# Kernel tuning notes

Measured on AMD Instinct MI355X. Metric: run time of the kernel, lower is better.

## Reference

```python
import jax, jax.numpy as jnp
import numpy as np

H, D = 8, 16            # num_heads, head_size
IN = H * D              # hgt_in_dim = 128
NT, ET = 3, 4           # node types, edge types (hard-coded in module)
N_DRUG, N_DIS, N_PROT = 10000, 10000, 30000
N = N_DRUG + N_DIS + N_PROT
E = 400000
LAYERS = 2
SQRT_D = float(np.sqrt(D))

# homogeneous node-type vector (presorted by type, as dgl.to_homogeneous yields)
NTYPE = jnp.concatenate([
    jnp.zeros(N_DRUG, jnp.int32),
    jnp.ones(N_DIS, jnp.int32),
    jnp.full((N_PROT,), 2, jnp.int32),
])


def typed_linear(x, types, W):
    # x: (M, in), W: (T, in, out), types: (M,) -> y[m] = x[m] @ W[types[m]]
    out = jnp.zeros((x.shape[0], W.shape[2]), x.dtype)
    for t in range(W.shape[0]):
        out = out + jnp.where((types == t)[:, None], x @ W[t], 0.0)
    return out


def hgt_conv(x, src, dst, etype, Wk, Wq, Wv, Wa, rel_att, rel_msg, pri, skip):
    # type-specific K/Q/V projections
    k = typed_linear(x, NTYPE, Wk).reshape(N, H, D)
    q = typed_linear(x, NTYPE, Wq).reshape(N, H, D)
    v = typed_linear(x, NTYPE, Wv).reshape(N, H, D)
    ke, qe, ve = k[src], q[dst], v[src]          # (E, H, D) gathers

    # per-edge-type relation transforms (vectorized over heads)
    kw = jnp.zeros_like(ke)
    mw = jnp.zeros_like(ve)
    for t in range(ET):
        sel = (etype == t)[:, None, None]
        kw = kw + jnp.where(sel, jnp.einsum('ehd,hdo->eho', ke, rel_att[:, t]), 0.0)
        mw = mw + jnp.where(sel, jnp.einsum('ehd,hdo->eho', ve, rel_msg[:, t]), 0.0)

    # attention logits: (kw . q) * relation_pri[head, etype] / sqrt(D)
    a = (kw * qe).sum(-1) * pri.T[etype] / SQRT_D  # (E, H)

    # edge softmax grouped by destination node, per head
    amax = jax.ops.segment_max(a, dst, num_segments=N)      # (N, H)
    ea = jnp.exp(a - amax[dst])
    esum = jax.ops.segment_sum(ea, dst, num_segments=N)
    attn = ea / esum[dst]                                   # (E, H)

    # weighted message aggregation (scatter-add over dst)
    m = mw * attn[..., None]                                 # (E, H, D)
    h = jax.ops.segment_sum(m, dst, num_segments=N).reshape(N, IN)

    # output projection (dropout = identity in eval) + sigmoid-skip residual
    h = typed_linear(h, NTYPE, Wa)
    alpha = jax.nn.sigmoid(skip)[NTYPE][:, None]
    return h * alpha + x * (1.0 - alpha)


def setup_inputs() -> dict:
    key = jax.random.key(0)
    ks = jax.random.split(key, 12)
    s = 0.05
    return {
        "drug_feature": jax.random.normal(ks[0], (N_DRUG, IN), jnp.float32),
        "disease_feature": jax.random.normal(ks[1], (N_DIS, IN), jnp.float32),
        "protein_feature": jax.random.normal(ks[2], (N_PROT, IN), jnp.float32),
        "src": jax.random.randint(ks[3], (E,), 0, N, dtype=jnp.int32),
        "dst": jax.random.randint(ks[4], (E,), 0, N, dtype=jnp.int32),
        "etype": jnp.sort(jax.random.randint(ks[5], (E,), 0, ET, dtype=jnp.int32)),
        "Wk": jax.random.normal(ks[6], (NT, IN, IN), jnp.float32) * s,
        "Wq": jax.random.normal(ks[7], (NT, IN, IN), jnp.float32) * s,
        "Wv": jax.random.normal(ks[8], (NT, IN, IN), jnp.float32) * s,
        "Wa": jax.random.normal(ks[9], (NT, IN, IN), jnp.float32) * s,
        "rel_att": jax.random.normal(ks[10], (H, ET, D, D), jnp.float32) * 0.1,
        "rel_msg": jax.random.normal(ks[11], (H, ET, D, D), jnp.float32) * 0.1,
        "pri": jnp.ones((H, ET), jnp.float32),
        "skip": jnp.ones((NT,), jnp.float32),
    }


def reference(drug_feature, disease_feature, protein_feature, src, dst, etype,
              Wk, Wq, Wv, Wa, rel_att, rel_msg, pri, skip):
    x = jnp.concatenate([drug_feature, disease_feature, protein_feature], axis=0)
    # ModuleList holds the SAME conv instance -> shared weights across layers
    for _ in range(LAYERS):
        x = hgt_conv(x, src, dst, etype, Wk, Wq, Wv, Wa, rel_att, rel_msg, pri, skip)
    return x
```

## Files before the change

### kernel.cpp

```cpp
#include <hip/hip_runtime.h>

#define N_NODE 50000
#define N_EDGE 400000
#define INF    128

#define FUSED_BLOCKS 1024

#define TILES0 313
#define TILES1 313
#define TILES2 938
#define PTILES 1564
#define PBLOCKS 391

#define SB_CONCAT 2048
#define SB_COUNT  1563
#define SB_TWT    768
#define SB_TRMSG  32
#define SB_TOTAL  (SB_CONCAT + SB_COUNT + SB_TWT + SB_TRMSG)

typedef __bf16 bf16x8 __attribute__((ext_vector_type(8)));
typedef float  f32x4  __attribute__((ext_vector_type(4)));

__device__ __forceinline__ void seg_decode(int b, int& ty, int& base, int& nrows) {
  if (b < TILES0)            { ty = 0; base = b * 32;                      nrows = 10000 - base; }
  else if (b < TILES0+TILES1){ ty = 1; base = 10000 + (b - TILES0) * 32;   nrows = 20000 - base; }
  else                       { ty = 2; base = 20000 + (b - TILES0-TILES1)*32; nrows = 50000 - base; }
  if (nrows > 32) nrows = 32;
}

__device__ __forceinline__ float blo(unsigned u) { return __uint_as_float(u << 16); }
__device__ __forceinline__ float bhi(unsigned u) { return __uint_as_float(u & 0xffff0000u); }
__device__ __forceinline__ unsigned bpack(float lo, float hi) {
  unsigned a = __float_as_uint(lo), b = __float_as_uint(hi);
  a = (a + 0x7fffu + ((a >> 16) & 1u)) >> 16;
  b = (b + 0x7fffu + ((b >> 16) & 1u)) & 0xffff0000u;
  return a | b;
}
__device__ __forceinline__ unsigned short b16(float v) {
  unsigned u = __float_as_uint(v);
  return (unsigned short)((u + 0x7fffu + ((u >> 16) & 1u)) >> 16);
}
__device__ __forceinline__ bf16x8 ld_frag(const unsigned short* p) {
  uint4 u = *reinterpret_cast<const uint4*>(p);
  return __builtin_bit_cast(bf16x8, u);
}

__global__ __launch_bounds__(256) void k_setup(const float* __restrict__ dr,
                                               const float* __restrict__ di,
                                               const float* __restrict__ pr,
                                               float* __restrict__ x,
                                               unsigned short* __restrict__ xh,
                                               const int* __restrict__ dst,
                                               int* __restrict__ deg,
                                               const float* __restrict__ Wk,
                                               const float* __restrict__ Wq,
                                               const float* __restrict__ Wv,
                                               const float* __restrict__ Wa,
                                               unsigned short* __restrict__ WT,
                                               const float* __restrict__ rm,
                                               float* __restrict__ AmT) {
  int b = blockIdx.x;
  if (b < SB_CONCAT) {
    for (int i = b * 256 + threadIdx.x; i < N_NODE * 32; i += SB_CONCAT * 256) {
      int row = i >> 5;
      float4 val;
      if (row < 10000)      val = ((const float4*)dr)[i];
      else if (row < 20000) val = ((const float4*)di)[i - 10000*32];
      else                  val = ((const float4*)pr)[i - 20000*32];
      ((float4*)x)[i] = val;
      ((uint2*)xh)[i] = make_uint2(bpack(val.x, val.y), bpack(val.z, val.w));
    }
  } else if (b < SB_CONCAT + SB_COUNT) {
    int e = (b - SB_CONCAT) * 256 + threadIdx.x;
    if (e < N_EDGE) atomicAdd(&deg[dst[e]], 1);
  } else if (b < SB_CONCAT + SB_COUNT + SB_TWT) {
    int idx = (b - SB_CONCAT - SB_COUNT) * 256 + threadIdx.x;
    if (idx < 196608) {
      int mt = idx >> 14;
      int within = idx & 16383;
      int o = within >> 7, ii = within & 127;
      int mat = mt / 3, ty = mt % 3;
      const float* W = (mat == 0) ? Wk : (mat == 1) ? Wq : (mat == 2) ? Wv : Wa;
      WT[idx] = b16(W[ty * 16384 + ii * 128 + o]);
    }
  } else {
    int i = (b - SB_CONCAT - SB_COUNT - SB_TWT) * 256 + threadIdx.x;
    int di2 = i & 15, doo = (i >> 4) & 15, ty = (i >> 8) & 3, hh = i >> 10;
    AmT[i] = rm[((hh * 4 + ty) * 16 + di2) * 16 + doo];
  }
}

__global__ __launch_bounds__(1024) void k_scan(const int* __restrict__ deg,
                                               int* __restrict__ off, int* __restrict__ cur) {
  __shared__ int part[1024];
  int t = threadIdx.x;
  int c0 = t * 49;
  int c1 = c0 + 49; if (c1 > N_NODE) c1 = N_NODE;
  int s = 0;
  for (int i = c0; i < c1; ++i) s += deg[i];
  part[t] = s;
  __syncthreads();
  for (int ofs = 1; ofs < 1024; ofs <<= 1) {
    int v = (t >= ofs) ? part[t - ofs] : 0;
    __syncthreads();
    part[t] += v;
    __syncthreads();
  }
  int run = (t == 0) ? 0 : part[t - 1];
  for (int i = c0; i < c1; ++i) { off[i] = run; cur[i] = run; run += deg[i]; }
  if (t == 1023) off[N_NODE] = part[1023];
}

__global__ __launch_bounds__(256) void k_fill(const int* __restrict__ dst,
                                              const int* __restrict__ src,
                                              const int* __restrict__ etp,
                                              int* __restrict__ cur, int* __restrict__ est) {
  int e = blockIdx.x * 256 + threadIdx.x;
  if (e < N_EDGE) {
    int p = atomicAdd(&cur[dst[e]], 1);
    est[p] = (src[e] << 2) | etp[e];
  } else if (e < N_EDGE + 64) {
    est[e] = 0;
  }
}

__global__ __launch_bounds__(256) void k_qkv(const unsigned short* __restrict__ xh,
                                             const unsigned short* __restrict__ WT,
                                             const float* __restrict__ rel_att,
                                             const float* __restrict__ pri,
                                             uint2* __restrict__ kvb,
                                             uint4* __restrict__ qab) {
  __shared__ unsigned short qsh[4][32][128];
  int w = threadIdx.x >> 6, l = threadIdx.x & 63;
  int r16 = l & 15, ks = l >> 4;
  int tile = blockIdx.x * 4 + w;
  int ty, base, wrows;
  seg_decode(tile, ty, base, wrows);
  int row0 = base;

  bf16x8 a[2][4];
#pragma unroll
  for (int st = 0; st < 2; ++st) {
    const unsigned short* xrow = xh + (size_t)(row0 + st * 16 + r16) * 128 + ks * 8;
#pragma unroll
    for (int kk = 0; kk < 4; ++kk) a[st][kk] = ld_frag(xrow + kk * 32);
  }

  const unsigned short* WK = WT + (size_t)(0 * 3 + ty) * 16384;
  const unsigned short* WQ = WT + (size_t)(1 * 3 + ty) * 16384;
  const unsigned short* WV = WT + (size_t)(2 * 3 + ty) * 16384;

#pragma unroll 1
  for (int ct = 0; ct < 8; ++ct) {
    int o = ct * 16 + r16;
    bf16x8 fbk[4], fbq[4], fbv[4];
#pragma unroll
    for (int kk = 0; kk < 4; ++kk) {
      fbk[kk] = ld_frag(WK + (size_t)o * 128 + ks * 8 + kk * 32);
      fbq[kk] = ld_frag(WQ + (size_t)o * 128 + ks * 8 + kk * 32);
      fbv[kk] = ld_frag(WV + (size_t)o * 128 + ks * 8 + kk * 32);
    }
#pragma unroll
    for (int st = 0; st < 2; ++st) {
      f32x4 ak = {0.f,0.f,0.f,0.f}, aq = {0.f,0.f,0.f,0.f}, av = {0.f,0.f,0.f,0.f};
#pragma unroll
      for (int kk = 0; kk < 4; ++kk) {
        ak = __builtin_amdgcn_mfma_f32_16x16x32_bf16(a[st][kk], fbk[kk], ak, 0, 0, 0);
        aq = __builtin_amdgcn_mfma_f32_16x16x32_bf16(a[st][kk], fbq[kk], aq, 0, 0, 0);
        av = __builtin_amdgcn_mfma_f32_16x16x32_bf16(a[st][kk], fbv[kk], av, 0, 0, 0);
      }
#pragma unroll
      for (int r = 0; r < 4; ++r) {
        int rrel = st * 16 + ks * 4 + r;
        float kn = __shfl_xor(ak[r], 1);
        float vn = __shfl_xor(av[r], 1);
        qsh[w][rrel][o] = b16(aq[r]);
        if (rrel < wrows && (l & 1) == 0) {
          size_t p = (size_t)(row0 + rrel);
          kvb[p * 64 + (o >> 1)] = make_uint2(bpack(ak[r], kn), bpack(av[r], vn));
        }
      }
    }
  }

  int h = l >> 3, j = l & 7;
  float4 prh = ((const float4*)pri)[h];
  float prs[4] = { prh.x * 0.25f, prh.y * 0.25f, prh.z * 0.25f, prh.w * 0.25f };
  for (int nd = 0; nd < wrows; ++nd) {
    unsigned u[8];
    *(uint4*)&u[0] = *(uint4*)&qsh[w][nd][h * 16 + 0];
    *(uint4*)&u[4] = *(uint4*)&qsh[w][nd][h * 16 + 8];
    float qf[16];
#pragma unroll
    for (int q2 = 0; q2 < 8; ++q2) { qf[2*q2] = blo(u[q2]); qf[2*q2+1] = bhi(u[q2]); }
    unsigned pk[4];
#pragma unroll
    for (int t4 = 0; t4 < 4; ++t4) {
      const float* Ar = rel_att + (((h * 4 + t4) * 16) + 2 * j) * 16;
      float ax = 0.f, ay = 0.f;
#pragma unroll
      for (int o = 0; o < 16; ++o) {
        ax += Ar[o] * qf[o];
        ay += Ar[16 + o] * qf[o];
      }
      pk[t4] = bpack(ax * prs[t4], ay * prs[t4]);
    }
    qab[(size_t)(row0 + nd) * 64 + l] = make_uint4(pk[0], pk[1], pk[2], pk[3]);
  }
}

__global__ __launch_bounds__(256)
__attribute__((amdgpu_waves_per_eu(4, 4)))
void k_fused(const uint2* __restrict__ kvb,
             const uint4* __restrict__ qab,
             const int* __restrict__ off,
             const int* __restrict__ est,
             const float* __restrict__ AmT,
             unsigned* __restrict__ hbh) {
  __shared__ float accs[4][4][128];
  int w = threadIdx.x >> 6, l = threadIdx.x & 63;
  int h = l >> 3, j = l & 7;

  for (int n = blockIdx.x * 4 + w; n < N_NODE; n += FUSED_BLOCKS * 4) {
    int o0 = off[n], o1 = off[n + 1];

    uint4 qu = qab[(size_t)n * 64 + l];
    float2 qa0 = make_float2(blo(qu.x), bhi(qu.x));
    float2 qa1 = make_float2(blo(qu.y), bhi(qu.y));
    float2 qa2 = make_float2(blo(qu.z), bhi(qu.z));
    float2 qa3 = make_float2(blo(qu.w), bhi(qu.w));

    float ssum = 0.f;
    float2 z = make_float2(0.f, 0.f);
    float2 at0 = z, at1 = z, at2 = z, at3 = z;

#define PROC(KV, TY, VALID) { \
    int ty = (TY) & 3; \
    float kx = blo((KV).x), ky = bhi((KV).x); \
    float2 qat = (ty==0)?qa0:(ty==1)?qa1:(ty==2)?qa2:qa3; \
    float part = kx*qat.x + ky*qat.y; \
    part += __shfl_xor(part, 1); \
    part += __shfl_xor(part, 2); \
    part += __shfl_xor(part, 4); \
    float wgt = (VALID) ? __expf(part) : 0.f; \
    ssum += wgt; \
    float vx = blo((KV).y), vy = bhi((KV).y); \
    float w0=(ty==0)?wgt:0.f, w1=(ty==1)?wgt:0.f, w2=(ty==2)?wgt:0.f, w3=(ty==3)?wgt:0.f; \
    at0.x += w0*vx; at0.y += w0*vy; \
    at1.x += w1*vx; at1.y += w1*vy; \
    at2.x += w2*vx; at2.y += w2*vy; \
    at3.x += w3*vx; at3.y += w3*vy; }

    for (int b0 = o0; b0 < o1; b0 += 64) {
      int cnt = o1 - b0; if (cnt > 64) cnt = 64;
      int stv = est[b0 + (l < cnt ? l : cnt - 1)];
      int t0 = __shfl(stv, 0);
      int t1 = __shfl(stv, 1 < cnt ? 1 : 0);
      uint2 kv0 = kvb[(size_t)(t0 >> 2) * 64 + l];
      uint2 kv1 = kvb[(size_t)(t1 >> 2) * 64 + l];
      for (int i = 0; i < cnt; i += 2) {
        bool more = (i + 2) < cnt;
        int n0 = 0, n1 = 0; uint2 kn0, kn1;
        if (more) {
          n0 = __shfl(stv, i + 2);
          n1 = __shfl(stv, (i + 3) < cnt ? (i + 3) : (i + 2));
          kn0 = kvb[(size_t)(n0 >> 2) * 64 + l];
          kn1 = kvb[(size_t)(n1 >> 2) * 64 + l];
        }
        PROC(kv0, t0, true)
        PROC(kv1, t1, (i + 1) < cnt)
        if (more) { t0 = n0; t1 = n1; kv0 = kn0; kv1 = kn1; }
      }
    }
#undef PROC

    float inv = (ssum > 0.f) ? 1.f / ssum : 0.f;
    at0.x *= inv; at0.y *= inv;
    at1.x *= inv; at1.y *= inv;
    at2.x *= inv; at2.y *= inv;
    at3.x *= inv; at3.y *= inv;

    ((float2*)&accs[w][0][0])[l] = at0;
    ((float2*)&accs[w][1][0])[l] = at1;
    ((float2*)&accs[w][2][0])[l] = at2;
    ((float2*)&accs[w][3][0])[l] = at3;

    float ox = 0.f, oy = 0.f;
#pragma unroll
    for (int ty = 0; ty < 4; ++ty) {
      const float4* AmR = (const float4*)(AmT + ((h * 4 + ty) * 16) * 16);
#pragma unroll
      for (int d4 = 0; d4 < 4; ++d4) {
        float4 ac = *((float4*)&accs[w][ty][h * 16 + d4 * 4]);
        float4 m0 = AmR[(2 * j) * 4 + d4];
        float4 m1 = AmR[(2 * j + 1) * 4 + d4];
        ox += m0.x * ac.x + m0.y * ac.y + m0.z * ac.z + m0.w * ac.w;
        oy += m1.x * ac.x + m1.y * ac.y + m1.z * ac.z + m1.w * ac.w;
      }
    }
    hbh[(size_t)n * 64 + l] = bpack(ox, oy);
  }
}

__global__ __launch_bounds__(256) void k_outqkv(const unsigned short* __restrict__ hbh,
                                                const unsigned short* __restrict__ WT,
                                                const float* __restrict__ skipv,
                                                const float* __restrict__ rel_att,
                                                const float* __restrict__ pri,
                                                float* __restrict__ xio,
                                                uint2* __restrict__ kvb,
                                                uint4* __restrict__ qab) {
  __shared__ unsigned short qsh[4][32][136];
  int w = threadIdx.x >> 6, l = threadIdx.x & 63;
  int r16 = l & 15, ks = l >> 4;
  int tile = blockIdx.x * 4 + w;
  int ty, base, wrows;
  seg_decode(tile, ty, base, wrows);
  int row0 = base;

  {
    bf16x8 a[2][4];
#pragma unroll
    for (int st = 0; st < 2; ++st) {
      const unsigned short* hrow = hbh + (size_t)(row0 + st * 16 + r16) * 128 + ks * 8;
#pragma unroll
      for (int kk = 0; kk < 4; ++kk) a[st][kk] = ld_frag(hrow + kk * 32);
    }
    const unsigned short* WA = WT + (size_t)(3 * 3 + ty) * 16384;
    float alpha = 1.f / (1.f + __expf(-skipv[ty]));
    float beta = 1.f - alpha;
#pragma unroll 1
    for (int ct = 0; ct < 8; ++ct) {
      int o = ct * 16 + r16;
      bf16x8 ba[4];
#pragma unroll
      for (int kk = 0; kk < 4; ++kk)
        ba[kk] = ld_frag(WA + (size_t)o * 128 + ks * 8 + kk * 32);
#pragma unroll
      for (int st = 0; st < 2; ++st) {
        f32x4 acc = {0.f,0.f,0.f,0.f};
#pragma unroll
        for (int kk = 0; kk < 4; ++kk)
          acc = __builtin_amdgcn_mfma_f32_16x16x32_bf16(a[st][kk], ba[kk], acc, 0, 0, 0);
#pragma unroll
        for (int r = 0; r < 4; ++r) {
          int rrel = st * 16 + ks * 4 + r;
          size_t p = (size_t)(row0 + rrel) * 128 + o;
          float nx = 0.f;
          if (rrel < wrows) {
            nx = acc[r] * alpha + xio[p] * beta;
            xio[p] = nx;
          }
          qsh[w][rrel][o] = b16(nx);
        }
      }
    }
  }

  bf16x8 a[2][4];
#pragma unroll
  for (int st = 0; st < 2; ++st)
#pragma unroll
    for (int kk = 0; kk < 4; ++kk)
      a[st][kk] = ld_frag(&qsh[w][st * 16 + r16][ks * 8 + kk * 32]);

  const unsigned short* WK = WT + (size_t)(0 * 3 + ty) * 16384;
  const unsigned short* WQ = WT + (size_t)(1 * 3 + ty) * 16384;
  const unsigned short* WV = WT + (size_t)(2 * 3 + ty) * 16384;
#pragma unroll 1
  for (int ct = 0; ct < 8; ++ct) {
    int o = ct * 16 + r16;
    bf16x8 fbk[4], fbq[4], fbv[4];
#pragma unroll
    for (int kk = 0; kk < 4; ++kk) {
      fbk[kk] = ld_frag(WK + (size_t)o * 128 + ks * 8 + kk * 32);
      fbq[kk] = ld_frag(WQ + (size_t)o * 128 + ks * 8 + kk * 32);
      fbv[kk] = ld_frag(WV + (size_t)o * 128 + ks * 8 + kk * 32);
    }
#pragma unroll
    for (int st = 0; st < 2; ++st) {
      f32x4 ak = {0.f,0.f,0.f,0.f}, aq = {0.f,0.f,0.f,0.f}, av = {0.f,0.f,0.f,0.f};
#pragma unroll
      for (int kk = 0; kk < 4; ++kk) {
        ak = __builtin_amdgcn_mfma_f32_16x16x32_bf16(a[st][kk], fbk[kk], ak, 0, 0, 0);
        aq = __builtin_amdgcn_mfma_f32_16x16x32_bf16(a[st][kk], fbq[kk], aq, 0, 0, 0);
        av = __builtin_amdgcn_mfma_f32_16x16x32_bf16(a[st][kk], fbv[kk], av, 0, 0, 0);
      }
#pragma unroll
      for (int r = 0; r < 4; ++r) {
        int rrel = st * 16 + ks * 4 + r;
        float kn = __shfl_xor(ak[r], 1);
        float vn = __shfl_xor(av[r], 1);
        qsh[w][rrel][o] = b16(aq[r]);
        if (rrel < wrows && (l & 1) == 0) {
          size_t p = (size_t)(row0 + rrel);
          kvb[p * 64 + (o >> 1)] = make_uint2(bpack(ak[r], kn), bpack(av[r], vn));
        }
      }
    }
  }

  int h = l >> 3, j = l & 7;
  float4 prh = ((const float4*)pri)[h];
  float prs[4] = { prh.x * 0.25f, prh.y * 0.25f, prh.z * 0.25f, prh.w * 0.25f };
  for (int nd = 0; nd < wrows; ++nd) {
    unsigned u[8];
    *(uint4*)&u[0] = *(uint4*)&qsh[w][nd][h * 16 + 0];
    *(uint4*)&u[4] = *(uint4*)&qsh[w][nd][h * 16 + 8];
    float qf[16];
#pragma unroll
    for (int q2 = 0; q2 < 8; ++q2) { qf[2*q2] = blo(u[q2]); qf[2*q2+1] = bhi(u[q2]); }
    unsigned pk[4];
#pragma unroll
    for (int t4 = 0; t4 < 4; ++t4) {
      const float* Ar = rel_att + (((h * 4 + t4) * 16) + 2 * j) * 16;
      float ax = 0.f, ay = 0.f;
#pragma unroll
      for (int o = 0; o < 16; ++o) {
        ax += Ar[o] * qf[o];
        ay += Ar[16 + o] * qf[o];
      }
      pk[t4] = bpack(ax * prs[t4], ay * prs[t4]);
    }
    qab[(size_t)(row0 + nd) * 64 + l] = make_uint4(pk[0], pk[1], pk[2], pk[3]);
  }
}

__global__ __launch_bounds__(256) void k_out(const unsigned short* __restrict__ hbh,
                                             const unsigned short* __restrict__ WT,
                                             const float* __restrict__ skipv,
                                             float* __restrict__ xio) {
  int w = threadIdx.x >> 6, l = threadIdx.x & 63;
  int r16 = l & 15, ks = l >> 4;
  int tile = blockIdx.x * 4 + w;
  int ty, base, wrows;
  seg_decode(tile, ty, base, wrows);
  int row0 = base;

  bf16x8 a[2][4];
#pragma unroll
  for (int st = 0; st < 2; ++st) {
    const unsigned short* hrow = hbh + (size_t)(row0 + st * 16 + r16) * 128 + ks * 8;
#pragma unroll
    for (int kk = 0; kk < 4; ++kk) a[st][kk] = ld_frag(hrow + kk * 32);
  }

  const unsigned short* WA = WT + (size_t)(3 * 3 + ty) * 16384;
  float alpha = 1.f / (1.f + __expf(-skipv[ty]));
  float beta = 1.f - alpha;

#pragma unroll 1
  for (int ct = 0; ct < 8; ++ct) {
    int o = ct * 16 + r16;
    bf16x8 ba[4];
#pragma unroll
    for (int kk = 0; kk < 4; ++kk)
      ba[kk] = ld_frag(WA + (size_t)o * 128 + ks * 8 + kk * 32);
#pragma unroll
    for (int st = 0; st < 2; ++st) {
      f32x4 acc = {0.f,0.f,0.f,0.f};
#pragma unroll
      for (int kk = 0; kk < 4; ++kk)
        acc = __builtin_amdgcn_mfma_f32_16x16x32_bf16(a[st][kk], ba[kk], acc, 0, 0, 0);
#pragma unroll
      for (int r = 0; r < 4; ++r) {
        int rrel = st * 16 + ks * 4 + r;
        if (rrel < wrows) {
          size_t p = (size_t)(row0 + rrel) * 128 + o;
          xio[p] = acc[r] * alpha + xio[p] * beta;
        }
      }
    }
  }
}

extern "C" void kernel_launch(void* const* d_in, const int* in_sizes, int n_in,
                              void* d_out, int out_size, void* d_ws, size_t ws_size,
                              hipStream_t stream) {
  const float* drug = (const float*)d_in[0];
  const float* dis  = (const float*)d_in[1];
  const float* prot = (const float*)d_in[2];
  const int* src    = (const int*)d_in[3];
  const int* dst    = (const int*)d_in[4];
  const int* etp    = (const int*)d_in[5];
  const float* Wk   = (const float*)d_in[6];
  const float* Wq   = (const float*)d_in[7];
  const float* Wv   = (const float*)d_in[8];
  const float* Wa   = (const float*)d_in[9];
  const float* rel_att = (const float*)d_in[10];
  const float* rel_msg = (const float*)d_in[11];
  const float* pri  = (const float*)d_in[12];
  const float* skip = (const float*)d_in[13];
  float* x = (float*)d_out;

  char* w = (char*)d_ws;
  uint2*          kvb = (uint2*)(w + 0);
  unsigned*       hbh = (unsigned*)(w + 25600000);
  uint4*          qab = (uint4*)(w + 38400000);
  unsigned short* xh  = (unsigned short*)(w + 89600000);
  unsigned short* WT  = (unsigned short*)(w + 102400000);
  float*          AmT = (float*)(w + 102793216);
  int*            off = (int*)(w + 102825984);
  int*            est = (int*)(w + 103026048);
  int*            deg = (int*)(w + 25600000);
  int*            cur = (int*)(w + 25800064);

  (void)hipMemsetAsync(deg, 0, N_NODE * sizeof(int), stream);
  k_setup<<<SB_TOTAL, 256, 0, stream>>>(drug, dis, prot, x, xh, dst, deg,
                                        Wk, Wq, Wv, Wa, WT, rel_msg, AmT);
  k_scan<<<1, 1024, 0, stream>>>(deg, off, cur);
  k_fill<<<(N_EDGE + 64 + 255) / 256, 256, 0, stream>>>(dst, src, etp, cur, est);

  k_qkv<<<PBLOCKS, 256, 0, stream>>>(xh, WT, rel_att, pri, kvb, qab);
  k_fused<<<FUSED_BLOCKS, 256, 0, stream>>>(kvb, qab, off, est, AmT, hbh);
  k_outqkv<<<PBLOCKS, 256, 0, stream>>>((const unsigned short*)hbh, WT, skip,
                                        rel_att, pri, x, kvb, qab);
  k_fused<<<FUSED_BLOCKS, 256, 0, stream>>>(kvb, qab, off, est, AmT, hbh);
  k_out<<<PBLOCKS, 256, 0, stream>>>((const unsigned short*)hbh, WT, skip, x);
}
```

Before: 779.8 us.

## Split each projection tile across two waves and double block count

The projection kernels (k_qkv, k_outqkv, k_out) now assign two waves per 32-row tile, each handling half of the output column tiles and half of the rows in the rel_att post-pass, coordinated through shared memory and __syncthreads. The grid doubles from 391 to 782 blocks, so a GPU with many compute units gets more parallel work on a 1564-tile problem. Each wave still loads the full A fragments, so some global loads are duplicated, and the new block barriers add synchronisation. The fused kernel's waves_per_eu hint is also relaxed from (4,4) to (3,4), giving the compiler more register freedom.

```diff
diff --git a/kernel.cpp b/kernel.cpp
--- a/kernel.cpp
+++ b/kernel.cpp
@@ -10,7 +10,7 @@
 #define TILES1 313
 #define TILES2 938
 #define PTILES 1564
-#define PBLOCKS 391
+#define PBLOCKS2 782
 
 #define SB_CONCAT 2048
 #define SB_COUNT  1563
@@ -130,10 +130,11 @@
                                              const float* __restrict__ pri,
                                              uint2* __restrict__ kvb,
                                              uint4* __restrict__ qab) {
-  __shared__ unsigned short qsh[4][32][128];
+  __shared__ unsigned short qsh[2][32][136];
   int w = threadIdx.x >> 6, l = threadIdx.x & 63;
   int r16 = l & 15, ks = l >> 4;
-  int tile = blockIdx.x * 4 + w;
+  int t = w >> 1, ch = w & 1;
+  int tile = blockIdx.x * 2 + t;
   int ty, base, wrows;
   seg_decode(tile, ty, base, wrows);
   int row0 = base;
@@ -151,7 +152,7 @@
   const unsigned short* WV = WT + (size_t)(2 * 3 + ty) * 16384;
 
 #pragma unroll 1
-  for (int ct = 0; ct < 8; ++ct) {
+  for (int ct = ch * 4; ct < ch * 4 + 4; ++ct) {
     int o = ct * 16 + r16;
     bf16x8 fbk[4], fbq[4], fbv[4];
 #pragma unroll
@@ -174,7 +175,7 @@
         int rrel = st * 16 + ks * 4 + r;
         float kn = __shfl_xor(ak[r], 1);
         float vn = __shfl_xor(av[r], 1);
-        qsh[w][rrel][o] = b16(aq[r]);
+        qsh[t][rrel][o] = b16(aq[r]);
         if (rrel < wrows && (l & 1) == 0) {
           size_t p = (size_t)(row0 + rrel);
           kvb[p * 64 + (o >> 1)] = make_uint2(bpack(ak[r], kn), bpack(av[r], vn));
@@ -182,14 +183,18 @@
       }
     }
   }
+  __syncthreads();
 
   int h = l >> 3, j = l & 7;
   float4 prh = ((const float4*)pri)[h];
   float prs[4] = { prh.x * 0.25f, prh.y * 0.25f, prh.z * 0.25f, prh.w * 0.25f };
-  for (int nd = 0; nd < wrows; ++nd) {
+  int nd0 = ch * 16;
+  int lim = wrows - nd0; if (lim > 16) lim = 16;
+  for (int i = 0; i < lim; ++i) {
+    int nd = nd0 + i;
     unsigned u[8];
-    *(uint4*)&u[0] = *(uint4*)&qsh[w][nd][h * 16 + 0];
-    *(uint4*)&u[4] = *(uint4*)&qsh[w][nd][h * 16 + 8];
+    *(uint4*)&u[0] = *(uint4*)&qsh[t][nd][h * 16 + 0];
+    *(uint4*)&u[4] = *(uint4*)&qsh[t][nd][h * 16 + 8];
     float qf[16];
 #pragma unroll
     for (int q2 = 0; q2 < 8; ++q2) { qf[2*q2] = blo(u[q2]); qf[2*q2+1] = bhi(u[q2]); }
@@ -210,7 +215,7 @@
 }
 
 __global__ __launch_bounds__(256)
-__attribute__((amdgpu_waves_per_eu(4, 4)))
+__attribute__((amdgpu_waves_per_eu(3, 4)))
 void k_fused(const uint2* __restrict__ kvb,
              const uint4* __restrict__ qab,
              const int* __restrict__ off,
@@ -310,10 +315,11 @@
                                                 float* __restrict__ xio,
                                                 uint2* __restrict__ kvb,
                                                 uint4* __restrict__ qab) {
-  __shared__ unsigned short qsh[4][32][136];
+  __shared__ unsigned short qsh[2][32][136];
   int w = threadIdx.x >> 6, l = threadIdx.x & 63;
   int r16 = l & 15, ks = l >> 4;
-  int tile = blockIdx.x * 4 + w;
+  int t = w >> 1, ch = w & 1;
+  int tile = blockIdx.x * 2 + t;
   int ty, base, wrows;
   seg_decode(tile, ty, base, wrows);
   int row0 = base;
@@ -330,7 +336,7 @@
     float alpha = 1.f / (1.f + __expf(-skipv[ty]));
     float beta = 1.f - alpha;
 #pragma unroll 1
-    for (int ct = 0; ct < 8; ++ct) {
+    for (int ct = ch * 4; ct < ch * 4 + 4; ++ct) {
       int o = ct * 16 + r16;
       bf16x8 ba[4];
 #pragma unroll
@@ -351,24 +357,26 @@
             nx = acc[r] * alpha + xio[p] * beta;
             xio[p] = nx;
           }
-          qsh[w][rrel][o] = b16(nx);
+          qsh[t][rrel][o] = b16(nx);
         }
       }
     }
   }
+  __syncthreads();
 
   bf16x8 a[2][4];
 #pragma unroll
   for (int st = 0; st < 2; ++st)
 #pragma unroll
     for (int kk = 0; kk < 4; ++kk)
-      a[st][kk] = ld_frag(&qsh[w][st * 16 + r16][ks * 8 + kk * 32]);
+      a[st][kk] = ld_frag(&qsh[t][st * 16 + r16][ks * 8 + kk * 32]);
+  __syncthreads();
 
   const unsigned short* WK = WT + (size_t)(0 * 3 + ty) * 16384;
   const unsigned short* WQ = WT + (size_t)(1 * 3 + ty) * 16384;
   const unsigned short* WV = WT + (size_t)(2 * 3 + ty) * 16384;
 #pragma unroll 1
-  for (int ct = 0; ct < 8; ++ct) {
+  for (int ct = ch * 4; ct < ch * 4 + 4; ++ct) {
     int o = ct * 16 + r16;
     bf16x8 fbk[4], fbq[4], fbv[4];
 #pragma unroll
@@ -391,7 +399,7 @@
         int rrel = st * 16 + ks * 4 + r;
         float kn = __shfl_xor(ak[r], 1);
         float vn = __shfl_xor(av[r], 1);
-        qsh[w][rrel][o] = b16(aq[r]);
+        qsh[t][rrel][o] = b16(aq[r]);
         if (rrel < wrows && (l & 1) == 0) {
           size_t p = (size_t)(row0 + rrel);
           kvb[p * 64 + (o >> 1)] = make_uint2(bpack(ak[r], kn), bpack(av[r], vn));
@@ -399,14 +407,18 @@
       }
     }
   }
+  __syncthreads();
 
   int h = l >> 3, j = l & 7;
   float4 prh = ((const float4*)pri)[h];
   float prs[4] = { prh.x * 0.25f, prh.y * 0.25f, prh.z * 0.25f, prh.w * 0.25f };
-  for (int nd = 0; nd < wrows; ++nd) {
+  int nd0 = ch * 16;
+  int lim = wrows - nd0; if (lim > 16) lim = 16;
+  for (int i = 0; i < lim; ++i) {
+    int nd = nd0 + i;
     unsigned u[8];
-    *(uint4*)&u[0] = *(uint4*)&qsh[w][nd][h * 16 + 0];
-    *(uint4*)&u[4] = *(uint4*)&qsh[w][nd][h * 16 + 8];
+    *(uint4*)&u[0] = *(uint4*)&qsh[t][nd][h * 16 + 0];
+    *(uint4*)&u[4] = *(uint4*)&qsh[t][nd][h * 16 + 8];
     float qf[16];
 #pragma unroll
     for (int q2 = 0; q2 < 8; ++q2) { qf[2*q2] = blo(u[q2]); qf[2*q2+1] = bhi(u[q2]); }
@@ -432,7 +444,8 @@
                                              float* __restrict__ xio) {
   int w = threadIdx.x >> 6, l = threadIdx.x & 63;
   int r16 = l & 15, ks = l >> 4;
-  int tile = blockIdx.x * 4 + w;
+  int t = w >> 1, ch = w & 1;
+  int tile = blockIdx.x * 2 + t;
   int ty, base, wrows;
   seg_decode(tile, ty, base, wrows);
   int row0 = base;
@@ -450,7 +463,7 @@
   float beta = 1.f - alpha;
 
 #pragma unroll 1
-  for (int ct = 0; ct < 8; ++ct) {
+  for (int ct = ch * 4; ct < ch * 4 + 4; ++ct) {
     int o = ct * 16 + r16;
     bf16x8 ba[4];
 #pragma unroll
@@ -511,10 +524,10 @@
   k_scan<<<1, 1024, 0, stream>>>(deg, off, cur);
   k_fill<<<(N_EDGE + 64 + 255) / 256, 256, 0, stream>>>(dst, src, etp, cur, est);
 
-  k_qkv<<<PBLOCKS, 256, 0, stream>>>(xh, WT, rel_att, pri, kvb, qab);
+  k_qkv<<<PBLOCKS2, 256, 0, stream>>>(xh, WT, rel_att, pri, kvb, qab);
   k_fused<<<FUSED_BLOCKS, 256, 0, stream>>>(kvb, qab, off, est, AmT, hbh);
-  k_outqkv<<<PBLOCKS, 256, 0, stream>>>((const unsigned short*)hbh, WT, skip,
-                                        rel_att, pri, x, kvb, qab);
+  k_outqkv<<<PBLOCKS2, 256, 0, stream>>>((const unsigned short*)hbh, WT, skip,
+                                         rel_att, pri, x, kvb, qab);
   k_fused<<<FUSED_BLOCKS, 256, 0, stream>>>(kvb, qab, off, est, AmT, hbh);
-  k_out<<<PBLOCKS, 256, 0, stream>>>((const unsigned short*)hbh, WT, skip, x);
-}
+  k_out<<<PBLOCKS2, 256, 0, stream>>>((const unsigned short*)hbh, WT, skip, x);
+}
```

Measured after the change: 769.5 us. Within noise of the previous version (-1.3%).
